# Performance work log

Hardware: AMD Instinct MI355X
Metric: run time of the kernel (lower is better)

## Reference

```python
import jax, jax.numpy as jnp
import numpy as np

N = 40000       # nodes
E = 400000      # directed edges (before self-loops)
F_IN = 50       # PPI num_features
HID = 64        # per-head hidden
H = 4           # heads
NCLS = 121      # PPI num_classes
NEG_SLOPE = 0.2


def gat_layer(x, src, dst, W, a_src, a_dst, W_res, b, concat):
    """PyG GATConv: per-edge attention, segment softmax over dst, scatter-add."""
    n = x.shape[0]
    h, c = a_src.shape
    feat = (x @ W).reshape(n, h, c)                       # [N,H,C]
    al_s = (feat * a_src[None]).sum(-1)                   # [N,H]
    al_d = (feat * a_dst[None]).sum(-1)                   # [N,H]
    e = jax.nn.leaky_relu(al_s[src] + al_d[dst], NEG_SLOPE)  # [E,H]
    m = jax.ops.segment_max(e, dst, num_segments=n)       # stable softmax max
    e = jnp.exp(e - m[dst])
    denom = jax.ops.segment_sum(e, dst, num_segments=n)
    w = e / (denom[dst] + 1e-16)                          # [E,H] attention
    msg = feat[src] * w[:, :, None]                       # [E,H,C]
    out = jax.ops.segment_sum(msg, dst, num_segments=n)   # [N,H,C]
    out = out.reshape(n, h * c) if concat else out.mean(axis=1)
    return out + x @ W_res + b                            # residual proj + bias


def setup_inputs() -> dict:
    key = jax.random.key(0)
    ks = jax.random.split(key, 18)
    g = lambda k, shape: jax.random.normal(k, shape, dtype=jnp.float32) * 0.1
    return {
        "x": jax.random.normal(ks[0], (N, F_IN), dtype=jnp.float32),
        "edge_index": jax.random.randint(ks[1], (2, E), 0, N, dtype=jnp.int32),
        "W1": g(ks[2], (F_IN, H * HID)), "a1s": g(ks[3], (H, HID)), "a1d": g(ks[4], (H, HID)),
        "Wr1": g(ks[5], (F_IN, H * HID)), "b1": jnp.zeros((H * HID,), jnp.float32),
        "W2": g(ks[6], (H * HID, H * HID)), "a2s": g(ks[7], (H, HID)), "a2d": g(ks[8], (H, HID)),
        "Wr2": g(ks[9], (H * HID, H * HID)), "b2": jnp.zeros((H * HID,), jnp.float32),
        "W3": g(ks[10], (H * HID, H * NCLS)), "a3s": g(ks[11], (H, NCLS)), "a3d": g(ks[12], (H, NCLS)),
        "Wr3": g(ks[13], (H * HID, NCLS)), "b3": jnp.zeros((NCLS,), jnp.float32),
    }


def reference(x, edge_index, W1, a1s, a1d, Wr1, b1, W2, a2s, a2d, Wr2, b2,
              W3, a3s, a3d, Wr3, b3):
    loop = jnp.arange(N, dtype=edge_index.dtype)          # add_self_loops=True
    src = jnp.concatenate([edge_index[0], loop])
    dst = jnp.concatenate([edge_index[1], loop])
    h = jax.nn.relu(gat_layer(x, src, dst, W1, a1s, a1d, Wr1, b1, True))
    h = jax.nn.relu(gat_layer(h, src, dst, W2, a2s, a2d, Wr2, b2, True))
    return gat_layer(h, src, dst, W3, a3s, a3d, Wr3, b3, False)
```

## Files before the change

kernel.cpp:

```cpp
#include <hip/hip_runtime.h>
#include <hip/hip_bf16.h>


#define NNODES 40000
#define MPAD   40064
#define NEDGES 400000
#define FIN    50
#define NHEAD  4
#define SCANB  157
#define N4     160000

typedef __attribute__((ext_vector_type(8))) short short8;
typedef __attribute__((ext_vector_type(4))) float float4v;
typedef __attribute__((ext_vector_type(2))) float float2v;
typedef __attribute__((ext_vector_type(4))) unsigned short ushort4v;
typedef __attribute__((ext_vector_type(8))) unsigned short ushort8v;
typedef __attribute__((ext_vector_type(2))) unsigned int uint2v;
typedef __attribute__((ext_vector_type(4))) unsigned int uint4v;

__device__ inline unsigned short f2bf(float f) {
    union { float f; unsigned u; } v; v.f = f;
    unsigned r = v.u + 0x7fff + ((v.u >> 16) & 1);
    return (unsigned short)(r >> 16);
}
__device__ inline float bf2f(unsigned short u) {
    union { unsigned u; float f; } v; v.u = ((unsigned)u) << 16; return v.f;
}
__device__ inline float lrelu(float x) { return x >= 0.f ? x : 0.2f * x; }

typedef __attribute__((address_space(3))) unsigned int lds_u32;
typedef __attribute__((address_space(1))) const unsigned int glb_u32;
__device__ __forceinline__ void gl2lds16(const short* g, short* l) {
    __builtin_amdgcn_global_load_lds((glb_u32*)g, (lds_u32*)l, 16, 0, 0);
}

__global__ void hist_kernel(const int* __restrict__ dst, int* __restrict__ counts, int E) {
    int i = blockIdx.x * blockDim.x + threadIdx.x;
    if (i < E) atomicAdd(&counts[dst[i]], 1);
}

__global__ __launch_bounds__(256) void scan_local(const int* __restrict__ counts,
                                                  int* __restrict__ offsets,
                                                  int* __restrict__ partials) {
    __shared__ int sh[256];
    int b = blockIdx.x, t = threadIdx.x, i = b * 256 + t;
    int v = (i < NNODES) ? counts[i] : 0;
    sh[t] = v;
    __syncthreads();
    #pragma unroll
    for (int off = 1; off < 256; off <<= 1) {
        int u = (t >= off) ? sh[t - off] : 0;
        __syncthreads();
        sh[t] += u;
        __syncthreads();
    }
    if (i < NNODES) offsets[i] = sh[t] - v;
    if (t == 255) partials[b] = sh[255];
}

__global__ __launch_bounds__(256) void scan_partials(int* __restrict__ partials,
                                                     int* __restrict__ pexcl) {
    __shared__ int sh[256];
    int t = threadIdx.x;
    int v = (t < SCANB) ? partials[t] : 0;
    sh[t] = v;
    __syncthreads();
    #pragma unroll
    for (int off = 1; off < 256; off <<= 1) {
        int u = (t >= off) ? sh[t - off] : 0;
        __syncthreads();
        sh[t] += u;
        __syncthreads();
    }
    pexcl[t] = sh[t] - v;
}

__global__ __launch_bounds__(256) void scan_carry(int* __restrict__ offsets,
                                                  const int* __restrict__ pexcl) {
    int b = blockIdx.x, i = b * 256 + threadIdx.x;
    if (i < NNODES) offsets[i] += pexcl[b];
}

__global__ void scatter_kernel(const int* __restrict__ src, const int* __restrict__ dst,
                               int* __restrict__ offsets,
                               int* __restrict__ csr_src, int E) {
    int i = blockIdx.x * blockDim.x + threadIdx.x;
    if (i < E) {
        int d = dst[i];
        int pos = atomicAdd(&offsets[d], 1);
        csr_src[pos] = src[i];
    }
}

__global__ void convert_x(const float* __restrict__ x, short* __restrict__ xb) {
    int i = blockIdx.x * blockDim.x + threadIdx.x;
    if (i >= MPAD * 64) return;
    int r = i >> 6, k = i & 63;
    float v = (r < NNODES && k < FIN) ? x[r * FIN + k] : 0.f;
    xb[i] = f2bf(v);
}

__global__ void convert_pack1(const float* __restrict__ W1, const float* __restrict__ Wr1,
                              const float* __restrict__ W2, const float* __restrict__ Wr2,
                              short* __restrict__ wc1, short* __restrict__ wc2) {
    int i = blockIdx.x * blockDim.x + threadIdx.x;
    if (i < 32768) {
        const float* W = (i < 16384) ? W1 : Wr1;
        int j = i & 16383;
        int n = j >> 6, k = j & 63;
        wc1[i] = f2bf((k < FIN) ? W[k * 256 + n] : 0.f);
    } else if (i < 163840) {
        int j = (i - 32768) & 65535;
        const float* W = (i < 98304) ? W2 : Wr2;
        int n = j >> 8, k = j & 255;
        wc2[(i - 32768)] = f2bf(W[k * 256 + n]);
    }
}

__global__ void convert_pack2(const float* __restrict__ W3, const float* __restrict__ Wr3,
                              const float* __restrict__ a3s, const float* __restrict__ a3d,
                              short* __restrict__ wc3,
                              float* __restrict__ a3sp, float* __restrict__ a3dp) {
    int i = blockIdx.x * blockDim.x + threadIdx.x;
    if (i < 131072) {
        int j = i >> 8, k = i & 255;
        int h = j >> 7, c = j & 127;
        wc3[i] = f2bf((c < 121) ? W3[k * 484 + h * 121 + c] : 0.f);
    } else if (i < 163840) {
        int j = i - 131072;
        int n = j >> 8, k = j & 255;
        wc3[131072 + j] = f2bf((n < 121) ? Wr3[k * 121 + n] : 0.f);
    } else if (i < 164864) {
        int j = i - 163840;
        int which = j >> 9; int jj = j & 511;
        int h = jj >> 7, c = jj & 127;
        float v = (c < 121) ? (which ? a3d[h * 121 + c] : a3s[h * 121 + c]) : 0.f;
        (which ? a3dp : a3sp)[jj] = v;
    }
}

template<int MODE>
__global__ __launch_bounds__(256) void mfma_gemm_fused(const short* __restrict__ A,
                                                       const short* __restrict__ Bt,
                                                       const float* __restrict__ bias,
                                                       const float* __restrict__ asv,
                                                       const float* __restrict__ adv,
                                                       unsigned short* __restrict__ Fb,
                                                       unsigned short* __restrict__ Rb,
                                                       unsigned int* __restrict__ F8,
                                                       float* __restrict__ out,
                                                       float* __restrict__ al4,
                                                       int Kp) {
    const int NW  = MODE ? 512 : 256;
    const int NCB = MODE ? 5 : 4;
    __shared__ __align__(16) short AsBs[16384];
    __shared__ __align__(16) unsigned short Cs[2][32][132];
    short* As = AsBs;
    short* Bs = AsBs + 8192;

    const int tid = threadIdx.x;
    const int l   = tid & 63;
    const int w   = tid >> 6;
    const int wm  = w >> 1, wn = w & 1;
    const int lrow = l & 15;
    const int lq   = l >> 4;

    const int T = NCB * 313;
    const int flat = blockIdx.y * NCB + blockIdx.x;
    const int q8 = T >> 3, r8 = T & 7;
    const int xcd = flat & 7, sidx = flat >> 3;
    const int wg = (xcd < r8 ? xcd * (q8 + 1) : r8 * (q8 + 1) + (xcd - r8) * q8) + sidx;
    const int row0 = (wg / NCB) * 128;
    const int col0 = (wg % NCB) * 128;

    float4v acc[4][4] = {};

    const int lr_ld = tid >> 3;
    const int lk_ld = (tid & 7) * 8;
    const int nk = Kp >> 6;
    for (int t = 0; t < nk; ++t) {
        const int k0 = t << 6;
        if (t) __syncthreads();
        const size_t abase = (size_t)(row0 + lr_ld) * Kp + k0 + lk_ld;
        const size_t bbase = (size_t)(col0 + lr_ld) * Kp + k0 + lk_ld;
        #pragma unroll
        for (int j = 0; j < 4; ++j) {
            gl2lds16(&A[abase + (size_t)j * 32 * Kp],  &As[j * 2048 + tid * 8]);
            gl2lds16(&Bt[bbase + (size_t)j * 32 * Kp], &Bs[j * 2048 + tid * 8]);
        }
        __syncthreads();
        #pragma unroll
        for (int ks = 0; ks < 2; ++ks) {
            short8 aF[4], bF[4];
            #pragma unroll
            for (int rt = 0; rt < 4; ++rt)
                aF[rt] = *(const short8*)&As[(wm * 64 + rt * 16 + lrow) * 64 + ks * 32 + lq * 8];
            #pragma unroll
            for (int ct = 0; ct < 4; ++ct)
                bF[ct] = *(const short8*)&Bs[(wn * 64 + ct * 16 + lrow) * 64 + ks * 32 + lq * 8];
            #pragma unroll
            for (int rt = 0; rt < 4; ++rt)
                #pragma unroll
                for (int ct = 0; ct < 4; ++ct)
                    acc[rt][ct] = __builtin_amdgcn_mfma_f32_16x16x32_bf16(aF[rt], bF[ct],
                                                                          acc[rt][ct], 0, 0, 0);
        }
    }

    const int colbase = col0 + wn * 64;
    const bool isW = colbase < NW;

    if (isW) {
        const int head = (colbase * NHEAD) / NW;
        const int half = MODE ? ((colbase >> 6) & 1) : 0;
        float* als_o = al4 + (half ? 2 * N4 : 0);
        float* ald_o = als_o + N4;
        float as_c[4], ad_c[4];
        #pragma unroll
        for (int ct = 0; ct < 4; ++ct) {
            int col = colbase + ct * 16 + lrow;
            as_c[ct] = asv[col];
            ad_c[ct] = adv[col];
        }
        #pragma unroll
        for (int rt = 0; rt < 4; ++rt) {
            #pragma unroll
            for (int i = 0; i < 4; ++i) {
                int r = row0 + wm * 64 + rt * 16 + lq * 4 + i;
                float fs = 0.f, fd = 0.f;
                #pragma unroll
                for (int ct = 0; ct < 4; ++ct) {
                    float v = acc[rt][ct][i];
                    fs += v * as_c[ct];
                    fd += v * ad_c[ct];
                }
                #pragma unroll
                for (int o2 = 8; o2; o2 >>= 1) {
                    fs += __shfl_xor(fs, o2, 16);
                    fd += __shfl_xor(fd, o2, 16);
                }
                if (lrow == 0 && r < NNODES) {
                    als_o[r * 4 + head] = fs;
                    ald_o[r * 4 + head] = fd;
                }
            }
        }
    }

    const int rp = tid >> 2, g2 = rp >> 5, rr = rp & 31, qq = tid & 3;

    if (MODE == 1 && col0 >= 512) {
        float* Ls = (float*)AsBs;
        #pragma unroll
        for (int p = 0; p < 4; ++p) {
            __syncthreads();
            if (wm == (p >> 1)) {
                const int rt0 = (p & 1) * 2;
                #pragma unroll
                for (int rt2 = 0; rt2 < 2; ++rt2) {
                    int rt = rt0 + rt2;
                    #pragma unroll
                    for (int ct = 0; ct < 4; ++ct) {
                        int cl = wn * 64 + ct * 16 + lrow;
                        #pragma unroll
                        for (int i = 0; i < 4; ++i) {
                            int lr = rt2 * 16 + lq * 4 + i;
                            Ls[lr * 132 + cl] = acc[rt][ct][i];
                        }
                    }
                }
            }
            __syncthreads();
            #pragma unroll
            for (int it = 0; it < 16; ++it) {
                int idx = it * 256 + tid;
                int r = idx >> 7, c = idx & 127;
                int grow = row0 + p * 32 + r;
                if (c < 121 && grow < NNODES)
                    out[(size_t)grow * 121 + c] = Ls[r * 132 + c] + bias[c];
            }
        }
        return;
    }

    if (MODE == 1) {
        #pragma unroll
        for (int p = 0; p < 2; ++p) {
            if (p) __syncthreads();
            #pragma unroll
            for (int rt2 = 0; rt2 < 2; ++rt2) {
                int rt = p * 2 + rt2;
                #pragma unroll
                for (int ct = 0; ct < 4; ++ct) {
                    int cl = wn * 64 + ct * 16 + lrow;
                    #pragma unroll
                    for (int i = 0; i < 4; ++i) {
                        int lr = rt2 * 16 + lq * 4 + i;
                        Cs[wm][lr][cl] = f2bf(acc[rt][ct][i]);
                    }
                }
            }
            __syncthreads();
            int grow = row0 + g2 * 64 + p * 32 + rr;
            if (grow < NNODES) {
                #pragma unroll
                for (int k = 0; k < 4; ++k) {
                    ushort8v v = *(const ushort8v*)&Cs[g2][rr][qq * 32 + 8 * k];
                    int u0 = 0, u1 = 0;
                    u0 = __builtin_amdgcn_cvt_pk_fp8_f32(bf2f(v[0]), bf2f(v[1]), u0, false);
                    u0 = __builtin_amdgcn_cvt_pk_fp8_f32(bf2f(v[2]), bf2f(v[3]), u0, true);
                    u1 = __builtin_amdgcn_cvt_pk_fp8_f32(bf2f(v[4]), bf2f(v[5]), u1, false);
                    u1 = __builtin_amdgcn_cvt_pk_fp8_f32(bf2f(v[6]), bf2f(v[7]), u1, true);
                    uint2v wv; wv.x = (unsigned)u0; wv.y = (unsigned)u1;
                    *(uint2v*)&F8[(size_t)grow * 128 + (col0 >> 2) + qq * 8 + 2 * k] = wv;
                }
            }
        }
        return;
    }

    const bool isRb = col0 >= 256;
    unsigned short* dest = isRb ? Rb : Fb;
    const int cold = isRb ? col0 - 256 : col0;
    float badd[4] = {0.f, 0.f, 0.f, 0.f};
    if (isRb) {
        #pragma unroll
        for (int ct = 0; ct < 4; ++ct)
            badd[ct] = bias[col0 - 256 + wn * 64 + ct * 16 + lrow];
    }

    #pragma unroll
    for (int p = 0; p < 2; ++p) {
        if (p) __syncthreads();
        #pragma unroll
        for (int rt2 = 0; rt2 < 2; ++rt2) {
            int rt = p * 2 + rt2;
            #pragma unroll
            for (int ct = 0; ct < 4; ++ct) {
                int cl = wn * 64 + ct * 16 + lrow;
                #pragma unroll
                for (int i = 0; i < 4; ++i) {
                    int lr = rt2 * 16 + lq * 4 + i;
                    Cs[wm][lr][cl] = f2bf(acc[rt][ct][i] + badd[ct]);
                }
            }
        }
        __syncthreads();
        int grow = row0 + g2 * 64 + p * 32 + rr;
        if (grow < NNODES) {
            #pragma unroll
            for (int k = 0; k < 4; ++k) {
                ushort8v v = *(const ushort8v*)&Cs[g2][rr][qq * 32 + 8 * k];
                *(ushort8v*)&dest[(size_t)grow * 256 + cold + qq * 32 + 8 * k] = v;
            }
        }
    }
}

__global__ __launch_bounds__(256) void attn64_kernel(const unsigned short* __restrict__ featb,
                                                     const float* __restrict__ al4,
                                                     const int* __restrict__ offs,
                                                     const int* __restrict__ csr,
                                                     const unsigned short* __restrict__ Rb,
                                                     unsigned short* __restrict__ outb) {
    int n = blockIdx.x * 4 + (threadIdx.x >> 6);
    int l = threadIdx.x & 63;
    int half = l >> 5, li = l & 31;
    int h = li >> 3;
    int beg = n ? offs[n - 1] : 0;
    int end = offs[n];
    float d0 = al4[N4 + n * 4 + h];

    float a[8] = {};
    float s = 0.f;
    #pragma unroll 4
    for (int j = beg + half; j < end; j += 2) {
        int sn = csr[j];
        float p = __expf(lrelu(al4[sn * 4 + h] + d0));
        s += p;
        ushort8v f = *(const ushort8v*)&featb[(size_t)sn * 256 + 8 * li];
        #pragma unroll
        for (int i = 0; i < 8; ++i) a[i] += p * bf2f(f[i]);
    }
    s += __shfl_xor(s, 32, 64);
    #pragma unroll
    for (int i = 0; i < 8; ++i) a[i] += __shfl_xor(a[i], 32, 64);

    float p0 = __expf(lrelu(al4[n * 4 + h] + d0));
    s += p0;
    {
        ushort8v f = *(const ushort8v*)&featb[(size_t)n * 256 + 8 * li];
        #pragma unroll
        for (int i = 0; i < 8; ++i) a[i] += p0 * bf2f(f[i]);
    }
    if (half == 0) {
        float inv = 1.f / s;
        ushort8v r = *(const ushort8v*)&Rb[(size_t)n * 256 + 8 * li];
        ushort8v o;
        #pragma unroll
        for (int i = 0; i < 8; ++i) o[i] = f2bf(fmaxf(bf2f(r[i]) + a[i] * inv, 0.f));
        *(ushort8v*)&outb[(size_t)n * 256 + 8 * li] = o;
    }
}

__global__ __launch_bounds__(256) void attn121_kernel(const unsigned int* __restrict__ F8,
                                                      const float* __restrict__ al4,
                                                      const int* __restrict__ offs,
                                                      const int* __restrict__ csr,
                                                      float* __restrict__ out) {
    int n = blockIdx.x * 4 + (threadIdx.x >> 6);
    int l = threadIdx.x & 63;
    int half = l >> 5, li = l & 31;
    int h = li >> 3;
    int beg = n ? offs[n - 1] : 0;
    int end = offs[n];
    float dsum = al4[N4 + n * 4 + h] + al4[3 * N4 + n * 4 + h];

    float a[16] = {};
    float s = 0.f;
    #pragma unroll 2
    for (int j = beg + half; j < end; j += 2) {
        int sn = csr[j];
        float p = __expf(lrelu(al4[sn * 4 + h] + al4[2 * N4 + sn * 4 + h] + dsum));
        s += p;
        uint4v u = *(const uint4v*)&F8[(size_t)sn * 128 + 4 * li];
        #pragma unroll
        for (int k = 0; k < 4; ++k) {
            float2v lo = __builtin_amdgcn_cvt_pk_f32_fp8(u[k], false);
            float2v hi = __builtin_amdgcn_cvt_pk_f32_fp8(u[k], true);
            a[4 * k + 0] += p * lo.x; a[4 * k + 1] += p * lo.y;
            a[4 * k + 2] += p * hi.x; a[4 * k + 3] += p * hi.y;
        }
    }
    s += __shfl_xor(s, 32, 64);
    #pragma unroll
    for (int i = 0; i < 16; ++i) a[i] += __shfl_xor(a[i], 32, 64);

    float p0 = __expf(lrelu(al4[n * 4 + h] + al4[2 * N4 + n * 4 + h] + dsum));
    s += p0;
    {
        uint4v u = *(const uint4v*)&F8[(size_t)n * 128 + 4 * li];
        #pragma unroll
        for (int k = 0; k < 4; ++k) {
            float2v lo = __builtin_amdgcn_cvt_pk_f32_fp8(u[k], false);
            float2v hi = __builtin_amdgcn_cvt_pk_f32_fp8(u[k], true);
            a[4 * k + 0] += p0 * lo.x; a[4 * k + 1] += p0 * lo.y;
            a[4 * k + 2] += p0 * hi.x; a[4 * k + 3] += p0 * hi.y;
        }
    }
    float inv = 0.25f / s;
    #pragma unroll
    for (int i = 0; i < 16; ++i) {
        a[i] *= inv;
        a[i] += __shfl_xor(a[i], 8, 64);
        a[i] += __shfl_xor(a[i], 16, 64);
    }
    if (l < 8) {
        #pragma unroll
        for (int i = 0; i < 16; ++i) {
            int c = 16 * l + i;
            if (c < 121) out[(size_t)n * 121 + c] += a[i];
        }
    }
}

extern "C" void kernel_launch(void* const* d_in, const int* in_sizes, int n_in,
                              void* d_out, int out_size, void* d_ws, size_t ws_size,
                              hipStream_t stream) {
    const float* x   = (const float*)d_in[0];
    const int* ei    = (const int*)d_in[1];
    const float* W1  = (const float*)d_in[2];
    const float* a1s = (const float*)d_in[3];
    const float* a1d = (const float*)d_in[4];
    const float* Wr1 = (const float*)d_in[5];
    const float* b1  = (const float*)d_in[6];
    const float* W2  = (const float*)d_in[7];
    const float* a2s = (const float*)d_in[8];
    const float* a2d = (const float*)d_in[9];
    const float* Wr2 = (const float*)d_in[10];
    const float* b2  = (const float*)d_in[11];
    const float* W3  = (const float*)d_in[12];
    const float* a3s = (const float*)d_in[13];
    const float* a3d = (const float*)d_in[14];
    const float* Wr3 = (const float*)d_in[15];
    const float* b3  = (const float*)d_in[16];
    float* out = (float*)d_out;

    const int* e_src = ei;
    const int* e_dst = ei + NEDGES;

    char* ws = (char*)d_ws;
    size_t off = 0;
    auto carve = [&](size_t bytes) { void* p = ws + off; off += (bytes + 255) & ~255ull; return p; };
    unsigned short* Fb = (unsigned short*)carve((size_t)MPAD * 256 * 2);
    unsigned short* Rb = (unsigned short*)carve((size_t)MPAD * 256 * 2);
    unsigned short* Hb = (unsigned short*)carve((size_t)MPAD * 256 * 2);
    unsigned int* F8 = (unsigned int*)carve((size_t)NNODES * 128 * 4);
    short* xb   = (short*)carve((size_t)MPAD * 64 * 2);
    short* wc1  = (short*)carve((size_t)512 * 64 * 2);
    short* wc2  = (short*)carve((size_t)512 * 256 * 2);
    short* wc3  = (short*)carve((size_t)640 * 256 * 2);
    float* a3sp = (float*)carve(512 * 4);
    float* a3dp = (float*)carve(512 * 4);
    float* al4  = (float*)carve((size_t)4 * N4 * 4);
    int* csr_src = (int*)carve((size_t)NEDGES * 4);
    int* offsets = (int*)carve(((size_t)NNODES + 4) * 4);
    int* counts  = (int*)carve((size_t)NNODES * 4);
    int* partials = (int*)carve(256 * 4);
    int* pexcl    = (int*)carve(256 * 4);

    const int EB = (NEDGES + 255) / 256;
    dim3 blk(256);

    convert_x<<<(MPAD * 64 + 255) / 256, blk, 0, stream>>>(x, xb);
    convert_pack1<<<(163840 + 255) / 256, blk, 0, stream>>>(W1, Wr1, W2, Wr2, wc1, wc2);
    convert_pack2<<<(164864 + 255) / 256, blk, 0, stream>>>(W3, Wr3, a3s, a3d, wc3, a3sp, a3dp);

    hipMemsetAsync(counts, 0, NNODES * 4, stream);
    hist_kernel<<<EB, blk, 0, stream>>>(e_dst, counts, NEDGES);
    scan_local<<<SCANB, blk, 0, stream>>>(counts, offsets, partials);
    scan_partials<<<1, blk, 0, stream>>>(partials, pexcl);
    scan_carry<<<SCANB, blk, 0, stream>>>(offsets, pexcl);
    scatter_kernel<<<EB, blk, 0, stream>>>(e_src, e_dst, offsets, csr_src, NEDGES);

    mfma_gemm_fused<0><<<dim3(4, 313), blk, 0, stream>>>(xb, wc1, b1, a1s, a1d,
                                                         Fb, Rb, nullptr, nullptr, al4, 64);
    attn64_kernel<<<NNODES / 4, blk, 0, stream>>>(Fb, al4, offsets, csr_src, Rb, Hb);

    mfma_gemm_fused<0><<<dim3(4, 313), blk, 0, stream>>>((short*)Hb, wc2, b2, a2s, a2d,
                                                         Fb, Rb, nullptr, nullptr, al4, 256);
    attn64_kernel<<<NNODES / 4, blk, 0, stream>>>(Fb, al4, offsets, csr_src, Rb, Hb);

    mfma_gemm_fused<1><<<dim3(5, 313), blk, 0, stream>>>((short*)Hb, wc3, b3, a3sp, a3dp,
                                                         nullptr, nullptr, F8, out, al4, 256);
    attn121_kernel<<<NNODES / 4, blk, 0, stream>>>(F8, al4, offsets, csr_src, out);
}
```

Before: 384.4 us.

## Precompute per-edge attention weights and software-pipeline feature gathers in attention kernels

```diff
diff --git a/kernel.cpp b/kernel.cpp
--- a/kernel.cpp
+++ b/kernel.cpp
@@ -83,13 +83,38 @@
 
 __global__ void scatter_kernel(const int* __restrict__ src, const int* __restrict__ dst,
                                int* __restrict__ offsets,
-                               int* __restrict__ csr_src, int E) {
+                               int* __restrict__ csr_src, int* __restrict__ csr_dst, int E) {
     int i = blockIdx.x * blockDim.x + threadIdx.x;
     if (i < E) {
         int d = dst[i];
         int pos = atomicAdd(&offsets[d], 1);
         csr_src[pos] = src[i];
-    }
+        csr_dst[pos] = d;
+    }
+}
+
+template<int FULL>
+__global__ void edge_p(const float* __restrict__ al4,
+                       const int* __restrict__ csr_src, const int* __restrict__ csr_dst,
+                       float* __restrict__ p4, int E) {
+    int j = blockIdx.x * blockDim.x + threadIdx.x;
+    if (j >= E) return;
+    int s = csr_src[j], d = csr_dst[j];
+    float4v a0 = *(const float4v*)&al4[s * 4];
+    float4v b0 = *(const float4v*)&al4[N4 + d * 4];
+    float4v lg;
+    lg.x = a0.x + b0.x; lg.y = a0.y + b0.y; lg.z = a0.z + b0.z; lg.w = a0.w + b0.w;
+    if (FULL) {
+        float4v a1 = *(const float4v*)&al4[2 * N4 + s * 4];
+        float4v b1 = *(const float4v*)&al4[3 * N4 + d * 4];
+        lg.x += a1.x + b1.x; lg.y += a1.y + b1.y; lg.z += a1.z + b1.z; lg.w += a1.w + b1.w;
+    }
+    float4v p;
+    p.x = __expf(lrelu(lg.x));
+    p.y = __expf(lrelu(lg.y));
+    p.z = __expf(lrelu(lg.z));
+    p.w = __expf(lrelu(lg.w));
+    *(float4v*)&p4[(size_t)j * 4] = p;
 }
 
 __global__ void convert_x(const float* __restrict__ x, short* __restrict__ xb) {
@@ -361,6 +386,7 @@
                                                      const float* __restrict__ al4,
                                                      const int* __restrict__ offs,
                                                      const int* __restrict__ csr,
+                                                     const float* __restrict__ p4,
                                                      const unsigned short* __restrict__ Rb,
                                                      unsigned short* __restrict__ outb) {
     int n = blockIdx.x * 4 + (threadIdx.x >> 6);
@@ -369,24 +395,36 @@
     int h = li >> 3;
     int beg = n ? offs[n - 1] : 0;
     int end = offs[n];
-    float d0 = al4[N4 + n * 4 + h];
 
     float a[8] = {};
     float s = 0.f;
-    #pragma unroll 4
-    for (int j = beg + half; j < end; j += 2) {
-        int sn = csr[j];
-        float p = __expf(lrelu(al4[sn * 4 + h] + d0));
-        s += p;
-        ushort8v f = *(const ushort8v*)&featb[(size_t)sn * 256 + 8 * li];
-        #pragma unroll
-        for (int i = 0; i < 8; ++i) a[i] += p * bf2f(f[i]);
+
+    int j = beg + half;
+    int sn_n = 0;
+    ushort8v u_c = {};
+    float p_c = 0.f;
+    if (j < end) {
+        int sn_c = csr[j];
+        u_c = *(const ushort8v*)&featb[(size_t)sn_c * 256 + 8 * li];
+        p_c = p4[(size_t)j * 4 + h];
+    }
+    if (j + 2 < end) sn_n = csr[j + 2];
+
+    for (; j < end; j += 2) {
+        int j2 = j + 2;
+        int sn_nn = (j2 + 2 < end) ? csr[j2 + 2] : 0;
+        ushort8v u_n = *(const ushort8v*)&featb[(size_t)sn_n * 256 + 8 * li];
+        float p_n = p4[(size_t)j2 * 4 + h];
+        s += p_c;
+        #pragma unroll
+        for (int i = 0; i < 8; ++i) a[i] += p_c * bf2f(u_c[i]);
+        u_c = u_n; p_c = p_n; sn_n = sn_nn;
     }
     s += __shfl_xor(s, 32, 64);
     #pragma unroll
     for (int i = 0; i < 8; ++i) a[i] += __shfl_xor(a[i], 32, 64);
 
-    float p0 = __expf(lrelu(al4[n * 4 + h] + d0));
+    float p0 = __expf(lrelu(al4[n * 4 + h] + al4[N4 + n * 4 + h]));
     s += p0;
     {
         ushort8v f = *(const ushort8v*)&featb[(size_t)n * 256 + 8 * li];
@@ -407,6 +445,7 @@
                                                       const float* __restrict__ al4,
                                                       const int* __restrict__ offs,
                                                       const int* __restrict__ csr,
+                                                      const float* __restrict__ p4,
                                                       float* __restrict__ out) {
     int n = blockIdx.x * 4 + (threadIdx.x >> 6);
     int l = threadIdx.x & 63;
@@ -414,29 +453,42 @@
     int h = li >> 3;
     int beg = n ? offs[n - 1] : 0;
     int end = offs[n];
-    float dsum = al4[N4 + n * 4 + h] + al4[3 * N4 + n * 4 + h];
 
     float a[16] = {};
     float s = 0.f;
-    #pragma unroll 2
-    for (int j = beg + half; j < end; j += 2) {
-        int sn = csr[j];
-        float p = __expf(lrelu(al4[sn * 4 + h] + al4[2 * N4 + sn * 4 + h] + dsum));
-        s += p;
-        uint4v u = *(const uint4v*)&F8[(size_t)sn * 128 + 4 * li];
+
+    int j = beg + half;
+    int sn_n = 0;
+    uint4v u_c = {};
+    float p_c = 0.f;
+    if (j < end) {
+        int sn_c = csr[j];
+        u_c = *(const uint4v*)&F8[(size_t)sn_c * 128 + 4 * li];
+        p_c = p4[(size_t)j * 4 + h];
+    }
+    if (j + 2 < end) sn_n = csr[j + 2];
+
+    for (; j < end; j += 2) {
+        int j2 = j + 2;
+        int sn_nn = (j2 + 2 < end) ? csr[j2 + 2] : 0;
+        uint4v u_n = *(const uint4v*)&F8[(size_t)sn_n * 128 + 4 * li];
+        float p_n = p4[(size_t)j2 * 4 + h];
+        s += p_c;
         #pragma unroll
         for (int k = 0; k < 4; ++k) {
-            float2v lo = __builtin_amdgcn_cvt_pk_f32_fp8(u[k], false);
-            float2v hi = __builtin_amdgcn_cvt_pk_f32_fp8(u[k], true);
-            a[4 * k + 0] += p * lo.x; a[4 * k + 1] += p * lo.y;
-            a[4 * k + 2] += p * hi.x; a[4 * k + 3] += p * hi.y;
-        }
+            float2v lo = __builtin_amdgcn_cvt_pk_f32_fp8(u_c[k], false);
+            float2v hi = __builtin_amdgcn_cvt_pk_f32_fp8(u_c[k], true);
+            a[4 * k + 0] += p_c * lo.x; a[4 * k + 1] += p_c * lo.y;
+            a[4 * k + 2] += p_c * hi.x; a[4 * k + 3] += p_c * hi.y;
+        }
+        u_c = u_n; p_c = p_n; sn_n = sn_nn;
     }
     s += __shfl_xor(s, 32, 64);
     #pragma unroll
     for (int i = 0; i < 16; ++i) a[i] += __shfl_xor(a[i], 32, 64);
 
-    float p0 = __expf(lrelu(al4[n * 4 + h] + al4[2 * N4 + n * 4 + h] + dsum));
+    float p0 = __expf(lrelu(al4[n * 4 + h] + al4[2 * N4 + n * 4 + h]
+                            + al4[N4 + n * 4 + h] + al4[3 * N4 + n * 4 + h]));
     s += p0;
     {
         uint4v u = *(const uint4v*)&F8[(size_t)n * 128 + 4 * li];
@@ -503,7 +555,9 @@
     float* a3sp = (float*)carve(512 * 4);
     float* a3dp = (float*)carve(512 * 4);
     float* al4  = (float*)carve((size_t)4 * N4 * 4);
+    float* p4   = (float*)carve(((size_t)NEDGES * 4 + 64) * 4);
     int* csr_src = (int*)carve((size_t)NEDGES * 4);
+    int* csr_dst = (int*)carve((size_t)NEDGES * 4);
     int* offsets = (int*)carve(((size_t)NNODES + 4) * 4);
     int* counts  = (int*)carve((size_t)NNODES * 4);
     int* partials = (int*)carve(256 * 4);
@@ -521,17 +575,20 @@
     scan_local<<<SCANB, blk, 0, stream>>>(counts, offsets, partials);
     scan_partials<<<1, blk, 0, stream>>>(partials, pexcl);
     scan_carry<<<SCANB, blk, 0, stream>>>(offsets, pexcl);
-    scatter_kernel<<<EB, blk, 0, stream>>>(e_src, e_dst, offsets, csr_src, NEDGES);
+    scatter_kernel<<<EB, blk, 0, stream>>>(e_src, e_dst, offsets, csr_src, csr_dst, NEDGES);
 
     mfma_gemm_fused<0><<<dim3(4, 313), blk, 0, stream>>>(xb, wc1, b1, a1s, a1d,
                                                          Fb, Rb, nullptr, nullptr, al4, 64);
-    attn64_kernel<<<NNODES / 4, blk, 0, stream>>>(Fb, al4, offsets, csr_src, Rb, Hb);
+    edge_p<0><<<EB, blk, 0, stream>>>(al4, csr_src, csr_dst, p4, NEDGES);
+    attn64_kernel<<<NNODES / 4, blk, 0, stream>>>(Fb, al4, offsets, csr_src, p4, Rb, Hb);
 
     mfma_gemm_fused<0><<<dim3(4, 313), blk, 0, stream>>>((short*)Hb, wc2, b2, a2s, a2d,
                                                          Fb, Rb, nullptr, nullptr, al4, 256);
-    attn64_kernel<<<NNODES / 4, blk, 0, stream>>>(Fb, al4, offsets, csr_src, Rb, Hb);
+    edge_p<0><<<EB, blk, 0, stream>>>(al4, csr_src, csr_dst, p4, NEDGES);
+    attn64_kernel<<<NNODES / 4, blk, 0, stream>>>(Fb, al4, offsets, csr_src, p4, Rb, Hb);
 
     mfma_gemm_fused<1><<<dim3(5, 313), blk, 0, stream>>>((short*)Hb, wc3, b3, a3sp, a3dp,
                                                          nullptr, nullptr, F8, out, al4, 256);
-    attn121_kernel<<<NNODES / 4, blk, 0, stream>>>(F8, al4, offsets, csr_src, out);
-}
+    edge_p<1><<<EB, blk, 0, stream>>>(al4, csr_src, csr_dst, p4, NEDGES);
+    attn121_kernel<<<NNODES / 4, blk, 0, stream>>>(F8, al4, offsets, csr_src, p4, out);
+}
```

Result: slower. 406.6 us (+5.8%).

## Software-pipeline edge gather loops, alias GEMM shared memory, precombine layer-3 attention logits

Applied to the files above, without the earlier changes.

```diff
diff --git a/kernel.cpp b/kernel.cpp
--- a/kernel.cpp
+++ b/kernel.cpp
@@ -90,6 +90,17 @@
         int pos = atomicAdd(&offsets[d], 1);
         csr_src[pos] = src[i];
     }
+}
+
+__global__ void al_combine(float* __restrict__ al4) {
+    int i = blockIdx.x * blockDim.x + threadIdx.x;
+    if (i >= 80000) return;
+    float4v* dst; const float4v* src;
+    if (i < 40000) { dst = (float4v*)&al4[2 * N4] + i;            src = (const float4v*)&al4[0] + i; }
+    else           { dst = (float4v*)&al4[3 * N4] + (i - 40000);  src = (const float4v*)&al4[N4] + (i - 40000); }
+    float4v d = *dst, s0 = *src;
+    d.x += s0.x; d.y += s0.y; d.z += s0.z; d.w += s0.w;
+    *dst = d;
 }
 
 __global__ void convert_x(const float* __restrict__ x, short* __restrict__ xb) {
@@ -153,10 +164,11 @@
                                                        int Kp) {
     const int NW  = MODE ? 512 : 256;
     const int NCB = MODE ? 5 : 4;
-    __shared__ __align__(16) short AsBs[16384];
-    __shared__ __align__(16) unsigned short Cs[2][32][132];
-    short* As = AsBs;
-    short* Bs = AsBs + 8192;
+    __shared__ __align__(16) char smem[32768];
+    short* As = (short*)smem;
+    short* Bs = (short*)(smem + 16384);
+    auto Cs = (unsigned short (*)[32][132])smem;
+    float* Ls = (float*)smem;
 
     const int tid = threadIdx.x;
     const int l   = tid & 63;
@@ -250,7 +262,6 @@
     const int rp = tid >> 2, g2 = rp >> 5, rr = rp & 31, qq = tid & 3;
 
     if (MODE == 1 && col0 >= 512) {
-        float* Ls = (float*)AsBs;
         #pragma unroll
         for (int p = 0; p < 4; ++p) {
             __syncthreads();
@@ -286,7 +297,7 @@
     if (MODE == 1) {
         #pragma unroll
         for (int p = 0; p < 2; ++p) {
-            if (p) __syncthreads();
+            __syncthreads();
             #pragma unroll
             for (int rt2 = 0; rt2 < 2; ++rt2) {
                 int rt = p * 2 + rt2;
@@ -331,7 +342,7 @@
 
     #pragma unroll
     for (int p = 0; p < 2; ++p) {
-        if (p) __syncthreads();
+        __syncthreads();
         #pragma unroll
         for (int rt2 = 0; rt2 < 2; ++rt2) {
             int rt = p * 2 + rt2;
@@ -373,14 +384,28 @@
 
     float a[8] = {};
     float s = 0.f;
-    #pragma unroll 4
-    for (int j = beg + half; j < end; j += 2) {
-        int sn = csr[j];
-        float p = __expf(lrelu(al4[sn * 4 + h] + d0));
-        s += p;
-        ushort8v f = *(const ushort8v*)&featb[(size_t)sn * 256 + 8 * li];
-        #pragma unroll
-        for (int i = 0; i < 8; ++i) a[i] += p * bf2f(f[i]);
+
+    int j = beg + half;
+    int sn_n = 0;
+    ushort8v u_c = {};
+    float al_c = 0.f;
+    if (j < end) {
+        int sn_c = csr[j];
+        u_c = *(const ushort8v*)&featb[(size_t)sn_c * 256 + 8 * li];
+        al_c = al4[sn_c * 4 + h];
+    }
+    if (j + 2 < end) sn_n = csr[j + 2];
+
+    for (; j < end; j += 2) {
+        int j2 = j + 2;
+        int sn_nn = (j2 + 2 < end) ? csr[j2 + 2] : 0;
+        ushort8v u_n = *(const ushort8v*)&featb[(size_t)sn_n * 256 + 8 * li];
+        float al_n = al4[sn_n * 4 + h];
+        float p_c = __expf(lrelu(al_c + d0));
+        s += p_c;
+        #pragma unroll
+        for (int i = 0; i < 8; ++i) a[i] += p_c * bf2f(u_c[i]);
+        u_c = u_n; al_c = al_n; sn_n = sn_nn;
     }
     s += __shfl_xor(s, 32, 64);
     #pragma unroll
@@ -414,29 +439,43 @@
     int h = li >> 3;
     int beg = n ? offs[n - 1] : 0;
     int end = offs[n];
-    float dsum = al4[N4 + n * 4 + h] + al4[3 * N4 + n * 4 + h];
+    float dD = al4[3 * N4 + n * 4 + h];
 
     float a[16] = {};
     float s = 0.f;
-    #pragma unroll 2
-    for (int j = beg + half; j < end; j += 2) {
-        int sn = csr[j];
-        float p = __expf(lrelu(al4[sn * 4 + h] + al4[2 * N4 + sn * 4 + h] + dsum));
-        s += p;
-        uint4v u = *(const uint4v*)&F8[(size_t)sn * 128 + 4 * li];
+
+    int j = beg + half;
+    int sn_n = 0;
+    uint4v u_c = {};
+    float al_c = 0.f;
+    if (j < end) {
+        int sn_c = csr[j];
+        u_c = *(const uint4v*)&F8[(size_t)sn_c * 128 + 4 * li];
+        al_c = al4[2 * N4 + sn_c * 4 + h];
+    }
+    if (j + 2 < end) sn_n = csr[j + 2];
+
+    for (; j < end; j += 2) {
+        int j2 = j + 2;
+        int sn_nn = (j2 + 2 < end) ? csr[j2 + 2] : 0;
+        uint4v u_n = *(const uint4v*)&F8[(size_t)sn_n * 128 + 4 * li];
+        float al_n = al4[2 * N4 + sn_n * 4 + h];
+        float p_c = __expf(lrelu(al_c + dD));
+        s += p_c;
         #pragma unroll
         for (int k = 0; k < 4; ++k) {
-            float2v lo = __builtin_amdgcn_cvt_pk_f32_fp8(u[k], false);
-            float2v hi = __builtin_amdgcn_cvt_pk_f32_fp8(u[k], true);
-            a[4 * k + 0] += p * lo.x; a[4 * k + 1] += p * lo.y;
-            a[4 * k + 2] += p * hi.x; a[4 * k + 3] += p * hi.y;
-        }
+            float2v lo = __builtin_amdgcn_cvt_pk_f32_fp8(u_c[k], false);
+            float2v hi = __builtin_amdgcn_cvt_pk_f32_fp8(u_c[k], true);
+            a[4 * k + 0] += p_c * lo.x; a[4 * k + 1] += p_c * lo.y;
+            a[4 * k + 2] += p_c * hi.x; a[4 * k + 3] += p_c * hi.y;
+        }
+        u_c = u_n; al_c = al_n; sn_n = sn_nn;
     }
     s += __shfl_xor(s, 32, 64);
     #pragma unroll
     for (int i = 0; i < 16; ++i) a[i] += __shfl_xor(a[i], 32, 64);
 
-    float p0 = __expf(lrelu(al4[n * 4 + h] + al4[2 * N4 + n * 4 + h] + dsum));
+    float p0 = __expf(lrelu(al4[2 * N4 + n * 4 + h] + dD));
     s += p0;
     {
         uint4v u = *(const uint4v*)&F8[(size_t)n * 128 + 4 * li];
@@ -533,5 +572,6 @@
 
     mfma_gemm_fused<1><<<dim3(5, 313), blk, 0, stream>>>((short*)Hb, wc3, b3, a3sp, a3dp,
                                                          nullptr, nullptr, F8, out, al4, 256);
+    al_combine<<<313, blk, 0, stream>>>(al4);
     attn121_kernel<<<NNODES / 4, blk, 0, stream>>>(F8, al4, offsets, csr_src, out);
 }
```

Result: slower. 392.3 us (+2.0%).
